# Kernel optimization log

Measured on AMD Instinct MI355X. Metric: run time of the kernel, lower is better.

## Reference

```python
import jax, jax.numpy as jnp
import numpy as np

CMIN, CMAX = -1024.0, 1016.0  # clamp(min=-2**10, max=2**10 - 8) after every op
BRIGHT_F = 1.9   # 1.0 + linspace(0, 0.9, 11)[10]
COLOR_F = 1.9    # 1.0 + linspace(0, 0.9, 11)[10]


def _brightness_dct(x, f):
    # pixel-domain multiplicative brightness; DCT is linear -> scale all coeffs
    return x * f


def _contrast_dct(x, f):
    # pixel contrast: (p - mean)*f + mean.
    # In DCT: AC coeffs scale by f; DC coeff blends toward per-channel mean DC.
    dc_mean = jnp.mean(x[..., 0, 0], axis=(-2, -1), keepdims=True)  # [C,1,1]
    out = x * f
    out = out.at[..., 0, 0].add((1.0 - f) * dc_mean)
    return out


def setup_inputs() -> dict:
    key = jax.random.key(0)
    k1, k2 = jax.random.split(key)
    # luma: [C=1, Hblocks, Wblocks, 8, 8]; chroma 4:2:0: [C=2, H/2, W/2, 8, 8]
    y = jax.random.normal(k1, (1, 512, 512, 8, 8), dtype=jnp.float32) * 100.0
    c = jax.random.normal(k2, (2, 256, 256, 8, 8), dtype=jnp.float32) * 100.0
    return {"y": y, "c": c}


def reference(y, c):
    clamp = lambda t: jnp.clip(t, CMIN, CMAX)
    # dct_prep(mode='start') treated as identity; initial clamp as in forward()
    y = clamp(y)
    c = clamp(c)
    # op 1: Brightness on luma (coeff[0]); both planes clamped after each op
    y = clamp(_brightness_dct(y, BRIGHT_F))
    c = clamp(c)
    # op 2: Color = contrast on chroma (coeff[1])
    c = clamp(_contrast_dct(c, COLOR_F))
    y = clamp(y)
    # dct_prep(mode='end') treated as identity
    return y, c
```

## Files before the change

### kernel.cpp

```cpp
#include <hip/hip_runtime.h>

#define CMIN -1024.0f
#define CMAX 1016.0f

__device__ __forceinline__ float clampv(float x) {
    return fminf(fmaxf(x, CMIN), CMAX);
}

__device__ __forceinline__ float wave_reduce(float v) {
    #pragma unroll
    for (int off = 32; off > 0; off >>= 1)
        v += __shfl_down(v, off, 64);
    return v;
}

__device__ __forceinline__ float4 xform(float4 v) {
    float4 r;
    r.x = clampv(clampv(v.x) * 1.9f);
    r.y = clampv(clampv(v.y) * 1.9f);
    r.z = clampv(clampv(v.z) * 1.9f);
    r.w = clampv(clampv(v.w) * 1.9f);
    return r;
}


__global__ void __launch_bounds__(256)
payload(const float4* __restrict__ y4, const float4* __restrict__ c4,
        float4* __restrict__ out, float* __restrict__ partials,
        float* __restrict__ dcbuf, int yblocks, int ynvec)
{
    const int b = blockIdx.x;
    const int t = threadIdx.x;

    if (b < yblocks) {
        const int base = b * 1024 + t;
        float4 v0 = y4[base];
        float4 v1 = y4[base + 256];
        float4 v2 = y4[base + 512];
        float4 v3 = y4[base + 768];
        out[base]       = xform(v0);
        out[base + 256] = xform(v1);
        out[base + 512] = xform(v2);
        out[base + 768] = xform(v3);
        return;
    }

    const int cb   = b - yblocks;
    const int base = cb * 1024 + t;
    float4 v0 = c4[base];
    float4 v1 = c4[base + 256];
    float4 v2 = c4[base + 512];
    float4 v3 = c4[base + 768];

    const bool isDC = (t & 15) == 0;
    float part = 0.0f;
    if (isDC) {
        const int d0 = base >> 4;
        dcbuf[d0]      = clampv(v0.x) * 1.9f;
        dcbuf[d0 + 16] = clampv(v1.x) * 1.9f;
        dcbuf[d0 + 32] = clampv(v2.x) * 1.9f;
        dcbuf[d0 + 48] = clampv(v3.x) * 1.9f;
        part = clampv(v0.x) + clampv(v1.x) + clampv(v2.x) + clampv(v3.x);
    }

    out[ynvec + base]       = xform(v0);
    out[ynvec + base + 256] = xform(v1);
    out[ynvec + base + 512] = xform(v2);
    out[ynvec + base + 768] = xform(v3);

    __shared__ float sm[4];
    float s = wave_reduce(part);
    const int lane = t & 63;
    const int wave = t >> 6;
    if (lane == 0) sm[wave] = s;
    __syncthreads();
    if (t == 0) partials[cb] = sm[0] + sm[1] + sm[2] + sm[3];
}

__global__ void __launch_bounds__(256)
dc_fixup(float* __restrict__ outc, const float* __restrict__ partials,
         const float* __restrict__ dcbuf, int dc_per_ch,
         float neg09_inv_count)
{
    const int t = threadIdx.x;
    const int d = blockIdx.x * 256 + t;

    const float pre = dcbuf[d];

    float s0 = partials[t] + partials[t + 256] +
               partials[t + 512] + partials[t + 768];
    float s1 = partials[1024 + t] + partials[1280 + t] +
               partials[1536 + t] + partials[1792 + t];
    s0 = wave_reduce(s0);
    s1 = wave_reduce(s1);

    __shared__ float sm[8];
    __shared__ float sadj[2];
    const int lane = t & 63;
    const int wave = t >> 6;
    if (lane == 0) { sm[wave] = s0; sm[4 + wave] = s1; }
    __syncthreads();
    if (t == 0) {
        sadj[0] = (sm[0] + sm[1] + sm[2] + sm[3]) * neg09_inv_count;
        sadj[1] = (sm[4] + sm[5] + sm[6] + sm[7]) * neg09_inv_count;
    }
    __syncthreads();

    const float adj = (d < dc_per_ch) ? sadj[0] : sadj[1];
    outc[(size_t)d * 64] = clampv(pre + adj);
}

extern "C" void kernel_launch(void* const* d_in, const int* in_sizes, int n_in,
                              void* d_out, int out_size, void* d_ws, size_t ws_size,
                              hipStream_t stream) {
    const float* y = (const float*)d_in[0];
    const float* c = (const float*)d_in[1];
    float* out = (float*)d_out;
    float* ws  = (float*)d_ws;

    const int yN = in_sizes[0];
    const int cN = in_sizes[1];

    const int ynvec     = yN / 4;
    const int cnvec     = cN / 4;
    const int yblocks   = ynvec / 1024;
    const int cblocks   = cnvec / 1024;
    const int dc_count  = cN / 64;
    const int dc_per_ch = dc_count / 2;
    const float neg09_inv_count = -0.9f / (float)dc_per_ch;

    float* partials = ws;
    float* dcbuf    = ws + 2048;

    payload<<<yblocks + cblocks, 256, 0, stream>>>(
        (const float4*)y, (const float4*)c, (float4*)out, partials, dcbuf,
        yblocks, ynvec);

    dc_fixup<<<512, 256, 0, stream>>>(
        out + (size_t)yN, partials, dcbuf, dc_per_ch, neg09_inv_count);
}
```

Baseline: 181.4 us.

## Use fixed-grid kernel where every thread handles both luma and chroma slices

Replaces the per-plane block split with 2048 blocks in which each thread processes 8 strided luma float4s and 4 strided chroma float4s, with problem sizes hardcoded as constants. Chroma partial sums are split into two per-block partial arrays (one per channel half), so dc_fixup now reduces 2048 partials per channel. This cuts the block count and balances work across all blocks, but hardcodes input shapes and uses large-stride accesses per thread.

```diff
diff --git a/kernel.cpp b/kernel.cpp
--- a/kernel.cpp
+++ b/kernel.cpp
@@ -2,6 +2,12 @@
 
 #define CMIN -1024.0f
 #define CMAX 1016.0f
+
+#define YNVEC   4194304
+#define CNVEC   2097152
+#define NTHR    524288
+#define DCPJ    32768
+#define DC_PER_CH 65536
 
 __device__ __forceinline__ float clampv(float x) {
     return fminf(fmaxf(x, CMIN), CMAX);
@@ -27,70 +33,73 @@
 __global__ void __launch_bounds__(256)
 payload(const float4* __restrict__ y4, const float4* __restrict__ c4,
         float4* __restrict__ out, float* __restrict__ partials,
-        float* __restrict__ dcbuf, int yblocks, int ynvec)
+        float* __restrict__ dcbuf)
 {
-    const int b = blockIdx.x;
-    const int t = threadIdx.x;
+    const int t   = threadIdx.x;
+    const int tid = blockIdx.x * 256 + t;
 
-    if (b < yblocks) {
-        const int base = b * 1024 + t;
-        float4 v0 = y4[base];
-        float4 v1 = y4[base + 256];
-        float4 v2 = y4[base + 512];
-        float4 v3 = y4[base + 768];
-        out[base]       = xform(v0);
-        out[base + 256] = xform(v1);
-        out[base + 512] = xform(v2);
-        out[base + 768] = xform(v3);
-        return;
+    #pragma unroll
+    for (int k = 0; k < 2; ++k) {
+        const int g = tid + k * (4 * NTHR);
+        float4 a = y4[g];
+        float4 b = y4[g + NTHR];
+        float4 c = y4[g + 2 * NTHR];
+        float4 d = y4[g + 3 * NTHR];
+        out[g]            = xform(a);
+        out[g + NTHR]     = xform(b);
+        out[g + 2 * NTHR] = xform(c);
+        out[g + 3 * NTHR] = xform(d);
     }
 
-    const int cb   = b - yblocks;
-    const int base = cb * 1024 + t;
-    float4 v0 = c4[base];
-    float4 v1 = c4[base + 256];
-    float4 v2 = c4[base + 512];
-    float4 v3 = c4[base + 768];
+    float4 v0 = c4[tid];
+    float4 v1 = c4[tid + NTHR];
+    float4 v2 = c4[tid + 2 * NTHR];
+    float4 v3 = c4[tid + 3 * NTHR];
 
-    const bool isDC = (t & 15) == 0;
-    float part = 0.0f;
-    if (isDC) {
-        const int d0 = base >> 4;
-        dcbuf[d0]      = clampv(v0.x) * 1.9f;
-        dcbuf[d0 + 16] = clampv(v1.x) * 1.9f;
-        dcbuf[d0 + 32] = clampv(v2.x) * 1.9f;
-        dcbuf[d0 + 48] = clampv(v3.x) * 1.9f;
-        part = clampv(v0.x) + clampv(v1.x) + clampv(v2.x) + clampv(v3.x);
+    float s0 = 0.0f, s1 = 0.0f;
+    if ((t & 15) == 0) {
+        const int d0 = tid >> 4;
+        const float c0 = clampv(v0.x), c1 = clampv(v1.x);
+        const float c2 = clampv(v2.x), c3 = clampv(v3.x);
+        dcbuf[d0]            = c0 * 1.9f;
+        dcbuf[d0 + DCPJ]     = c1 * 1.9f;
+        dcbuf[d0 + 2 * DCPJ] = c2 * 1.9f;
+        dcbuf[d0 + 3 * DCPJ] = c3 * 1.9f;
+        s0 = c0 + c1;
+        s1 = c2 + c3;
     }
 
-    out[ynvec + base]       = xform(v0);
-    out[ynvec + base + 256] = xform(v1);
-    out[ynvec + base + 512] = xform(v2);
-    out[ynvec + base + 768] = xform(v3);
+    out[YNVEC + tid]            = xform(v0);
+    out[YNVEC + tid + NTHR]     = xform(v1);
+    out[YNVEC + tid + 2 * NTHR] = xform(v2);
+    out[YNVEC + tid + 3 * NTHR] = xform(v3);
 
-    __shared__ float sm[4];
-    float s = wave_reduce(part);
-    const int lane = t & 63;
-    const int wave = t >> 6;
-    if (lane == 0) sm[wave] = s;
+    __shared__ float sm0[4], sm1[4];
+    s0 = wave_reduce(s0);
+    s1 = wave_reduce(s1);
+    if ((t & 63) == 0) { sm0[t >> 6] = s0; sm1[t >> 6] = s1; }
     __syncthreads();
-    if (t == 0) partials[cb] = sm[0] + sm[1] + sm[2] + sm[3];
+    if (t == 0) {
+        partials[blockIdx.x]        = sm0[0] + sm0[1] + sm0[2] + sm0[3];
+        partials[2048 + blockIdx.x] = sm1[0] + sm1[1] + sm1[2] + sm1[3];
+    }
 }
 
 __global__ void __launch_bounds__(256)
 dc_fixup(float* __restrict__ outc, const float* __restrict__ partials,
-         const float* __restrict__ dcbuf, int dc_per_ch,
-         float neg09_inv_count)
+         const float* __restrict__ dcbuf, float neg09_inv_count)
 {
     const int t = threadIdx.x;
     const int d = blockIdx.x * 256 + t;
 
     const float pre = dcbuf[d];
 
-    float s0 = partials[t] + partials[t + 256] +
-               partials[t + 512] + partials[t + 768];
-    float s1 = partials[1024 + t] + partials[1280 + t] +
-               partials[1536 + t] + partials[1792 + t];
+    float s0 = 0.0f, s1 = 0.0f;
+    #pragma unroll
+    for (int j = 0; j < 2048; j += 256) {
+        s0 += partials[t + j];
+        s1 += partials[2048 + t + j];
+    }
     s0 = wave_reduce(s0);
     s1 = wave_reduce(s1);
 
@@ -106,7 +115,7 @@
     }
     __syncthreads();
 
-    const float adj = (d < dc_per_ch) ? sadj[0] : sadj[1];
+    const float adj = (d < DC_PER_CH) ? sadj[0] : sadj[1];
     outc[(size_t)d * 64] = clampv(pre + adj);
 }
 
@@ -118,24 +127,14 @@
     float* out = (float*)d_out;
     float* ws  = (float*)d_ws;
 
-    const int yN = in_sizes[0];
-    const int cN = in_sizes[1];
+    float* partials = ws;
+    float* dcbuf    = ws + 4096;
 
-    const int ynvec     = yN / 4;
-    const int cnvec     = cN / 4;
-    const int yblocks   = ynvec / 1024;
-    const int cblocks   = cnvec / 1024;
-    const int dc_count  = cN / 64;
-    const int dc_per_ch = dc_count / 2;
-    const float neg09_inv_count = -0.9f / (float)dc_per_ch;
+    const float neg09_inv_count = -0.9f / (float)DC_PER_CH;
 
-    float* partials = ws;
-    float* dcbuf    = ws + 2048;
-
-    payload<<<yblocks + cblocks, 256, 0, stream>>>(
-        (const float4*)y, (const float4*)c, (float4*)out, partials, dcbuf,
-        yblocks, ynvec);
+    payload<<<2048, 256, 0, stream>>>(
+        (const float4*)y, (const float4*)c, (float4*)out, partials, dcbuf);
 
     dc_fixup<<<512, 256, 0, stream>>>(
-        out + (size_t)yN, partials, dcbuf, dc_per_ch, neg09_inv_count);
+        out + (size_t)YNVEC * 4, partials, dcbuf, neg09_inv_count);
 }
```

Result: slower. 187.8 us (+3.6%).
